# Optimization experiments

Hardware: AMD Instinct MI355X
Metric: run time of the kernel (lower is better)

The kernel has to match this reference:

```python
import jax, jax.numpy as jnp
import numpy as np


def setup_inputs() -> dict:
    key = jax.random.key(0)
    x = jax.random.normal(key, (4, 256, 64, 64), dtype=jnp.float32)
    return {"x": x}


def reference(x):
    # x: [B, C, W, H]
    B, C, W, H = x.shape
    N = W * H
    q = x.reshape(B, C, N).transpose(0, 2, 1)  # [B, N, C] (proj_query)
    # per-token L2 norm over channels
    q_norm = jnp.linalg.norm(q, ord=2, axis=2)  # [B, N]
    # outer product of norms: [B, N, N]
    nm = q_norm[:, :, None] * q_norm[:, None, :]
    # raw dot-product energy: [B, N, N]
    energy = jnp.einsum('bnc,bmc->bnm', q, q)
    norm_energy = energy / (nm + 1e-6)
    attention = jax.nn.softmax(norm_energy, axis=-1)
    return attention
```

## Files before the change

kernel.cpp:

```cpp
#include <hip/hip_runtime.h>
#include <hip/hip_bf16.h>

#define BATCH 4
#define CDIM  256
#define NTOK  4096

#define BM 64
#define BN 128

typedef short bf16x8 __attribute__((ext_vector_type(8)));
typedef float floatx4 __attribute__((ext_vector_type(4)));
typedef unsigned int uintx4 __attribute__((ext_vector_type(4)));
typedef unsigned int u32;

#define PIN(v) asm volatile("" : "+v"(v))
#define WAIT(n) asm volatile("s_waitcnt vmcnt(" #n ")" ::: "memory")
#define BAR() do { __builtin_amdgcn_s_barrier(); asm volatile("" ::: "memory"); } while (0)

__device__ inline u32 f2bf1(float f) {
    u32 u = __float_as_uint(f);
    u += 0x7fffu + ((u >> 16) & 1u);
    return u >> 16;
}
__device__ inline u32 f2bf2(float lo, float hi) { return f2bf1(lo) | (f2bf1(hi) << 16); }

__device__ inline void gload_lds16(const short* g, short* l) {
    __builtin_amdgcn_global_load_lds(
        (const __attribute__((address_space(1))) u32*)g,
        (__attribute__((address_space(3))) u32*)l, 16, 0, 0);
}

#define TT 32
__global__ __launch_bounds__(256) void prep_kernel(const float* __restrict__ x,
                                                   short* __restrict__ xn) {
    __shared__ float tile[TT][CDIM + 2];
    __shared__ float part[8][TT];
    __shared__ float rinv_s[TT];
    const int tid = threadIdx.x;
    const int blk = blockIdx.x;
    const int b = blk >> 7;
    const int t0 = (blk & 127) * TT;
    const float* xb = x + (size_t)b * CDIM * NTOK;
    const int ti = tid & 31, cq = tid >> 5;
    float ss = 0.f;
    for (int c = cq; c < CDIM; c += 8) {
        float v = xb[(size_t)c * NTOK + t0 + ti];
        tile[ti][c] = v;
        ss += v * v;
    }
    part[cq][ti] = ss;
    __syncthreads();
    if (tid < TT) {
        float s = 0.f;
#pragma unroll
        for (int q = 0; q < 8; ++q) s += part[q][tid];
        rinv_s[tid] = 1.0f / sqrtf(s);
    }
    __syncthreads();
    const int tok = tid >> 3, seg = tid & 7;
    const float ri = rinv_s[tok];
    size_t obase = ((size_t)(b * NTOK + t0 + tok)) * CDIM + seg * 32;
#pragma unroll
    for (int j = 0; j < 4; ++j) {
        u32 w[4];
#pragma unroll
        for (int u = 0; u < 4; ++u) {
            float f0 = tile[tok][seg * 32 + j * 8 + 2 * u] * ri;
            float f1 = tile[tok][seg * 32 + j * 8 + 2 * u + 1] * ri;
            w[u] = f2bf2(f0, f1);
        }
        *(uintx4*)&xn[obase + j * 8] = (uintx4){w[0], w[1], w[2], w[3]};
    }
}

__global__ __launch_bounds__(512, 2) void attn_kernel(const short* __restrict__ xn,
                                                      float* __restrict__ out) {
    __shared__ short Bs[4][128][64];
    __shared__ float rowsumLds[BM][4];
    const int tid = threadIdx.x;
    const int D = blockIdx.x;
    const int b = D >> 6;
    const int rb = (D & 63) * BM;
    const short* xnb = xn + (size_t)b * NTOK * CDIM;
    float* outb = out + ((size_t)b << 24);
    const int lane = tid & 63, wid = tid >> 6;
    const int wr = (wid >> 2) * 32;
    const int wc = (wid & 3) * 32;
    const int r0 = lane & 15, kq = lane >> 4;
    const int sx = r0 & 7;
    const int tr0 = wc + r0, tr1 = wc + 16 + r0;

    const int trl0 = (wid << 3) + (lane >> 3);
    const int c8 = (lane & 7) ^ (lane >> 3);

    bf16x8 afr[2][8];
#pragma unroll
    for (int m = 0; m < 2; ++m) {
        const short* arow = xnb + (size_t)(rb + wr + m * 16 + r0) * CDIM;
#pragma unroll
        for (int j = 0; j < 8; ++j) {
            afr[m][j] = *(const bf16x8*)(arow + j * 32 + kq * 8);
            PIN(afr[m][j]);
        }
    }

    float psum0[4] = {0.f, 0.f, 0.f, 0.f}, psum1[4] = {0.f, 0.f, 0.f, 0.f};
    float rinv0[4], rinv1[4];
    floatx4 acc00, acc01, acc10, acc11;

    auto stage = [&](int ct, int kc) {
        const short* s0 = xnb + (size_t)(ct * BN + trl0) * CDIM + kc * 64 + c8 * 8;
        short* d = &Bs[kc][wid << 3][0];
        gload_lds16(s0, d);
        gload_lds16(s0 + (size_t)64 * CDIM, d + 64 * 64);
    };

#define ACCZERO() do { acc00 = (floatx4){0,0,0,0}; acc01 = (floatx4){0,0,0,0}; \
                       acc10 = (floatx4){0,0,0,0}; acc11 = (floatx4){0,0,0,0}; } while (0)

#define COMPUTE(KC) do { \
    __builtin_amdgcn_s_setprio(1); \
    const int p0 = kq ^ sx, p1 = (4 | kq) ^ sx; \
    bf16x8 b0a = *(const bf16x8*)&Bs[KC][tr0][p0 * 8]; \
    bf16x8 b1a = *(const bf16x8*)&Bs[KC][tr1][p0 * 8]; \
    bf16x8 b0b = *(const bf16x8*)&Bs[KC][tr0][p1 * 8]; \
    bf16x8 b1b = *(const bf16x8*)&Bs[KC][tr1][p1 * 8]; \
    acc00 = __builtin_amdgcn_mfma_f32_16x16x32_bf16(afr[0][(KC)*2],   b0a, acc00, 0,0,0); \
    acc10 = __builtin_amdgcn_mfma_f32_16x16x32_bf16(afr[1][(KC)*2],   b0a, acc10, 0,0,0); \
    acc01 = __builtin_amdgcn_mfma_f32_16x16x32_bf16(afr[0][(KC)*2],   b1a, acc01, 0,0,0); \
    acc11 = __builtin_amdgcn_mfma_f32_16x16x32_bf16(afr[1][(KC)*2],   b1a, acc11, 0,0,0); \
    acc00 = __builtin_amdgcn_mfma_f32_16x16x32_bf16(afr[0][(KC)*2+1], b0b, acc00, 0,0,0); \
    acc10 = __builtin_amdgcn_mfma_f32_16x16x32_bf16(afr[1][(KC)*2+1], b0b, acc10, 0,0,0); \
    acc01 = __builtin_amdgcn_mfma_f32_16x16x32_bf16(afr[0][(KC)*2+1], b1b, acc01, 0,0,0); \
    acc11 = __builtin_amdgcn_mfma_f32_16x16x32_bf16(afr[1][(KC)*2+1], b1b, acc11, 0,0,0); \
    __builtin_amdgcn_s_setprio(0); \
} while (0)

#define STEP(KC, SCT, SKC, WN) do { stage((SCT), (SKC)); WAIT(WN); BAR(); COMPUTE(KC); } while (0)
#define STEPNS(KC, WN)        do { WAIT(WN); BAR(); COMPUTE(KC); } while (0)

#define EPI0() do { \
    _Pragma("unroll") for (int r = 0; r < 4; ++r) { \
        psum0[r] += __expf(acc00[r] - 1.f) + __expf(acc01[r] - 1.f); \
        psum1[r] += __expf(acc10[r] - 1.f) + __expf(acc11[r] - 1.f); } \
} while (0)

#define EPI1(CT) do { \
    _Pragma("unroll") for (int r = 0; r < 4; ++r) { \
        const int row_a = rb + wr + kq * 4 + r; \
        float* pa = outb + ((size_t)row_a << 12) + ((CT) << 7) + wc + r0; \
        __builtin_nontemporal_store(__expf(acc00[r] - 1.f) * rinv0[r], pa); \
        __builtin_nontemporal_store(__expf(acc01[r] - 1.f) * rinv0[r], pa + 16); \
        float* pb = pa + ((size_t)16 << 12); \
        __builtin_nontemporal_store(__expf(acc10[r] - 1.f) * rinv1[r], pb); \
        __builtin_nontemporal_store(__expf(acc11[r] - 1.f) * rinv1[r], pb + 16); } \
} while (0)

    stage(0, 0); stage(0, 1);
    for (int ct = 0; ct < 31; ++ct) {
        ACCZERO();
        STEP(0, ct, 2, 4);
        STEP(1, ct, 3, 4);
        STEP(2, ct + 1, 0, 4);
        STEP(3, ct + 1, 1, 4);
        EPI0();
    }
    ACCZERO();
    STEP(0, 31, 2, 4);
    STEP(1, 31, 3, 4);
    STEPNS(2, 2);
    STEPNS(3, 0);
    EPI0();

#pragma unroll
    for (int r = 0; r < 4; ++r) {
        float v0 = psum0[r], v1 = psum1[r];
        v0 += __shfl_xor(v0, 1); v0 += __shfl_xor(v0, 2);
        v0 += __shfl_xor(v0, 4); v0 += __shfl_xor(v0, 8);
        v1 += __shfl_xor(v1, 1); v1 += __shfl_xor(v1, 2);
        v1 += __shfl_xor(v1, 4); v1 += __shfl_xor(v1, 8);
        if (r0 == 0) {
            rowsumLds[wr + kq * 4 + r][wid & 3] = v0;
            rowsumLds[wr + 16 + kq * 4 + r][wid & 3] = v1;
        }
    }
    __syncthreads();
#pragma unroll
    for (int r = 0; r < 4; ++r) {
        const int ra = wr + kq * 4 + r, rbw = wr + 16 + kq * 4 + r;
        rinv0[r] = 1.0f / (rowsumLds[ra][0] + rowsumLds[ra][1] + rowsumLds[ra][2] + rowsumLds[ra][3]);
        rinv1[r] = 1.0f / (rowsumLds[rbw][0] + rowsumLds[rbw][1] + rowsumLds[rbw][2] + rowsumLds[rbw][3]);
    }
    __syncthreads();

    stage(0, 0); stage(0, 1);
    {
        ACCZERO();
        STEP(0, 0, 2, 4);
        STEP(1, 0, 3, 4);
        STEP(2, 1, 0, 4);
        STEP(3, 1, 1, 4);
        EPI1(0);
    }
    for (int ct = 1; ct < 31; ++ct) {
        ACCZERO();
        STEP(0, ct, 2, 12);
        STEP(1, ct, 3, 12);
        STEP(2, ct + 1, 0, 4);
        STEP(3, ct + 1, 1, 4);
        EPI1(ct);
    }
    ACCZERO();
    STEP(0, 31, 2, 12);
    STEP(1, 31, 3, 12);
    STEPNS(2, 2);
    STEPNS(3, 0);
    EPI1(31);

#undef ACCZERO
#undef COMPUTE
#undef STEP
#undef STEPNS
#undef EPI0
#undef EPI1
}

extern "C" void kernel_launch(void* const* d_in, const int* in_sizes, int n_in,
                              void* d_out, int out_size, void* d_ws, size_t ws_size,
                              hipStream_t stream) {
    const float* x = (const float*)d_in[0];
    float* out = (float*)d_out;
    short* xn = (short*)d_ws;

    prep_kernel<<<BATCH * (NTOK / TT), 256, 0, stream>>>(x, xn);
    attn_kernel<<<NTOK / BM * BATCH, 512, 0, stream>>>(xn, out);
}
```

Baseline: 143.8 us.

## Stage attention output through LDS for coalesced stores and defer the epilogue by one tile

The second pass now writes the normalized exp values into a padded LDS tile. After a barrier, each wave reads rows of that tile and writes them with 16-byte nontemporal vector stores, replacing the scattered 4-byte global stores. The epilogue for each column tile is delayed by one iteration, using saved accumulators, and placed between MFMA steps of the next tile. The vmcnt wait counts are adjusted to account for the extra stores. The new ~33 KB LDS buffer raises per-block LDS use considerably, which may limit how many blocks fit per CU. It also adds an extra barrier and LDS round-trip per tile.

```diff
diff --git a/kernel.cpp b/kernel.cpp
--- a/kernel.cpp
+++ b/kernel.cpp
@@ -15,6 +15,7 @@
 
 #define PIN(v) asm volatile("" : "+v"(v))
 #define WAIT(n) asm volatile("s_waitcnt vmcnt(" #n ")" ::: "memory")
+#define LGKM0() asm volatile("s_waitcnt lgkmcnt(0)" ::: "memory")
 #define BAR() do { __builtin_amdgcn_s_barrier(); asm volatile("" ::: "memory"); } while (0)
 
 __device__ inline u32 f2bf1(float f) {
@@ -76,6 +77,7 @@
 __global__ __launch_bounds__(512, 2) void attn_kernel(const short* __restrict__ xn,
                                                       float* __restrict__ out) {
     __shared__ short Bs[4][128][64];
+    __shared__ float Co[64][132];
     __shared__ float rowsumLds[BM][4];
     const int tid = threadIdx.x;
     const int D = blockIdx.x;
@@ -107,6 +109,7 @@
     float psum0[4] = {0.f, 0.f, 0.f, 0.f}, psum1[4] = {0.f, 0.f, 0.f, 0.f};
     float rinv0[4], rinv1[4];
     floatx4 acc00, acc01, acc10, acc11;
+    floatx4 accP00, accP01, accP10, accP11;
 
     auto stage = [&](int ct, int kc) {
         const short* s0 = xnb + (size_t)(ct * BN + trl0) * CDIM + kc * 64 + c8 * 8;
@@ -117,6 +120,7 @@
 
 #define ACCZERO() do { acc00 = (floatx4){0,0,0,0}; acc01 = (floatx4){0,0,0,0}; \
                        acc10 = (floatx4){0,0,0,0}; acc11 = (floatx4){0,0,0,0}; } while (0)
+#define SAVEACC() do { accP00 = acc00; accP01 = acc01; accP10 = acc10; accP11 = acc11; } while (0)
 
 #define COMPUTE(KC) do { \
     __builtin_amdgcn_s_setprio(1); \
@@ -145,15 +149,20 @@
         psum1[r] += __expf(acc10[r] - 1.f) + __expf(acc11[r] - 1.f); } \
 } while (0)
 
-#define EPI1(CT) do { \
+#define SP(CT) do { \
     _Pragma("unroll") for (int r = 0; r < 4; ++r) { \
-        const int row_a = rb + wr + kq * 4 + r; \
-        float* pa = outb + ((size_t)row_a << 12) + ((CT) << 7) + wc + r0; \
-        __builtin_nontemporal_store(__expf(acc00[r] - 1.f) * rinv0[r], pa); \
-        __builtin_nontemporal_store(__expf(acc01[r] - 1.f) * rinv0[r], pa + 16); \
-        float* pb = pa + ((size_t)16 << 12); \
-        __builtin_nontemporal_store(__expf(acc10[r] - 1.f) * rinv1[r], pb); \
-        __builtin_nontemporal_store(__expf(acc11[r] - 1.f) * rinv1[r], pb + 16); } \
+        const int rowa = wr + kq * 4 + r; \
+        Co[rowa][wc + r0]           = __expf(accP00[r] - 1.f) * rinv0[r]; \
+        Co[rowa][wc + 16 + r0]      = __expf(accP01[r] - 1.f) * rinv0[r]; \
+        Co[rowa + 16][wc + r0]      = __expf(accP10[r] - 1.f) * rinv1[r]; \
+        Co[rowa + 16][wc + 16 + r0] = __expf(accP11[r] - 1.f) * rinv1[r]; } \
+    LGKM0(); \
+    BAR(); \
+    _Pragma("unroll") for (int p = 0; p < 4; ++p) { \
+        const int rw = (wid << 3) + (lane >> 5) + 2 * p; \
+        floatx4 v = *(const floatx4*)&Co[rw][(lane & 31) * 4]; \
+        __builtin_nontemporal_store(v, \
+            (floatx4*)(outb + (((size_t)(rb + rw)) << 12) + ((CT) << 7) + (lane & 31) * 4)); } \
 } while (0)
 
     stage(0, 0); stage(0, 1);
@@ -194,35 +203,37 @@
     __syncthreads();
 
     stage(0, 0); stage(0, 1);
-    {
-        ACCZERO();
-        STEP(0, 0, 2, 4);
-        STEP(1, 0, 3, 4);
-        STEP(2, 1, 0, 4);
-        STEP(3, 1, 1, 4);
-        EPI1(0);
-    }
+    ACCZERO();
+    STEP(0, 0, 2, 4);
+    STEP(1, 0, 3, 4);
+    STEP(2, 1, 0, 4);
+    STEP(3, 1, 1, 4);
+    SAVEACC();
     for (int ct = 1; ct < 31; ++ct) {
         ACCZERO();
-        STEP(0, ct, 2, 12);
-        STEP(1, ct, 3, 12);
-        STEP(2, ct + 1, 0, 4);
-        STEP(3, ct + 1, 1, 4);
-        EPI1(ct);
+        STEP(0, ct, 2, 4);
+        STEP(1, ct, 3, 4);
+        SP(ct - 1);
+        STEP(2, ct + 1, 0, 8);
+        STEP(3, ct + 1, 1, 8);
+        SAVEACC();
     }
     ACCZERO();
-    STEP(0, 31, 2, 12);
-    STEP(1, 31, 3, 12);
-    STEPNS(2, 2);
-    STEPNS(3, 0);
-    EPI1(31);
+    STEP(0, 31, 2, 4);
+    STEP(1, 31, 3, 4);
+    SP(30);
+    STEPNS(2, 6);
+    STEPNS(3, 4);
+    SAVEACC();
+    SP(31);
 
 #undef ACCZERO
+#undef SAVEACC
 #undef COMPUTE
 #undef STEP
 #undef STEPNS
 #undef EPI0
-#undef EPI1
+#undef SP
 }
 
 extern "C" void kernel_launch(void* const* d_in, const int* in_sizes, int n_in,
```

After: 145.5 us. About the same (+1.2%).

## Widen column tile to 256 with 1x8 warp layout covering all rows

Applied to the files above, without the earlier changes.

Doubles the column tile (BN 128→256) and reorganizes the eight warps so each one covers all 64 rows and a 32-column slice. Each warp now holds four A row-fragments in registers, so every B fragment read from LDS feeds four MFMAs instead of two, and the number of column-tile iterations per pass is halved. The cost is a 128 KB LDS B buffer and twice as many A registers, which likely prevents two blocks per CU despite the launch bounds. The row-sum reduction now spans eight warps, and the vmcnt waits are retuned for the larger stage and store counts.

```diff
diff --git a/kernel.cpp b/kernel.cpp
--- a/kernel.cpp
+++ b/kernel.cpp
@@ -6,7 +6,7 @@
 #define NTOK  4096
 
 #define BM 64
-#define BN 128
+#define BN 256
 
 typedef short bf16x8 __attribute__((ext_vector_type(8)));
 typedef float floatx4 __attribute__((ext_vector_type(4)));
@@ -75,8 +75,8 @@
 
 __global__ __launch_bounds__(512, 2) void attn_kernel(const short* __restrict__ xn,
                                                       float* __restrict__ out) {
-    __shared__ short Bs[4][128][64];
-    __shared__ float rowsumLds[BM][4];
+    __shared__ short Bs[4][256][64];
+    __shared__ float rowsumLds[BM][8];
     const int tid = threadIdx.x;
     const int D = blockIdx.x;
     const int b = D >> 6;
@@ -84,19 +84,18 @@
     const short* xnb = xn + (size_t)b * NTOK * CDIM;
     float* outb = out + ((size_t)b << 24);
     const int lane = tid & 63, wid = tid >> 6;
-    const int wr = (wid >> 2) * 32;
-    const int wc = (wid & 3) * 32;
+    const int wcol = wid << 5;
     const int r0 = lane & 15, kq = lane >> 4;
     const int sx = r0 & 7;
-    const int tr0 = wc + r0, tr1 = wc + 16 + r0;
-
-    const int trl0 = (wid << 3) + (lane >> 3);
+    const int tr0 = wcol + r0, tr1 = wcol + 16 + r0;
+
+    const int trl = (wid << 3) + (lane >> 3);
     const int c8 = (lane & 7) ^ (lane >> 3);
 
-    bf16x8 afr[2][8];
-#pragma unroll
-    for (int m = 0; m < 2; ++m) {
-        const short* arow = xnb + (size_t)(rb + wr + m * 16 + r0) * CDIM;
+    bf16x8 afr[4][8];
+#pragma unroll
+    for (int m = 0; m < 4; ++m) {
+        const short* arow = xnb + (size_t)(rb + m * 16 + r0) * CDIM;
 #pragma unroll
         for (int j = 0; j < 8; ++j) {
             afr[m][j] = *(const bf16x8*)(arow + j * 32 + kq * 8);
@@ -104,35 +103,37 @@
         }
     }
 
-    float psum0[4] = {0.f, 0.f, 0.f, 0.f}, psum1[4] = {0.f, 0.f, 0.f, 0.f};
-    float rinv0[4], rinv1[4];
-    floatx4 acc00, acc01, acc10, acc11;
+    float psum[16];
+#pragma unroll
+    for (int i = 0; i < 16; ++i) psum[i] = 0.f;
+    floatx4 acc[4][2];
 
     auto stage = [&](int ct, int kc) {
-        const short* s0 = xnb + (size_t)(ct * BN + trl0) * CDIM + kc * 64 + c8 * 8;
+        const short* s0 = xnb + (size_t)(ct * BN + trl) * CDIM + kc * 64 + c8 * 8;
         short* d = &Bs[kc][wid << 3][0];
-        gload_lds16(s0, d);
-        gload_lds16(s0 + (size_t)64 * CDIM, d + 64 * 64);
+#pragma unroll
+        for (int rr = 0; rr < 4; ++rr)
+            gload_lds16(s0 + (size_t)(rr * 64) * CDIM, d + rr * 64 * 64);
     };
 
-#define ACCZERO() do { acc00 = (floatx4){0,0,0,0}; acc01 = (floatx4){0,0,0,0}; \
-                       acc10 = (floatx4){0,0,0,0}; acc11 = (floatx4){0,0,0,0}; } while (0)
+#define ACCZERO() do { _Pragma("unroll") for (int m = 0; m < 4; ++m) { \
+        acc[m][0] = (floatx4){0,0,0,0}; acc[m][1] = (floatx4){0,0,0,0}; } } while (0)
 
 #define COMPUTE(KC) do { \
     __builtin_amdgcn_s_setprio(1); \
     const int p0 = kq ^ sx, p1 = (4 | kq) ^ sx; \
-    bf16x8 b0a = *(const bf16x8*)&Bs[KC][tr0][p0 * 8]; \
-    bf16x8 b1a = *(const bf16x8*)&Bs[KC][tr1][p0 * 8]; \
-    bf16x8 b0b = *(const bf16x8*)&Bs[KC][tr0][p1 * 8]; \
-    bf16x8 b1b = *(const bf16x8*)&Bs[KC][tr1][p1 * 8]; \
-    acc00 = __builtin_amdgcn_mfma_f32_16x16x32_bf16(afr[0][(KC)*2],   b0a, acc00, 0,0,0); \
-    acc10 = __builtin_amdgcn_mfma_f32_16x16x32_bf16(afr[1][(KC)*2],   b0a, acc10, 0,0,0); \
-    acc01 = __builtin_amdgcn_mfma_f32_16x16x32_bf16(afr[0][(KC)*2],   b1a, acc01, 0,0,0); \
-    acc11 = __builtin_amdgcn_mfma_f32_16x16x32_bf16(afr[1][(KC)*2],   b1a, acc11, 0,0,0); \
-    acc00 = __builtin_amdgcn_mfma_f32_16x16x32_bf16(afr[0][(KC)*2+1], b0b, acc00, 0,0,0); \
-    acc10 = __builtin_amdgcn_mfma_f32_16x16x32_bf16(afr[1][(KC)*2+1], b0b, acc10, 0,0,0); \
-    acc01 = __builtin_amdgcn_mfma_f32_16x16x32_bf16(afr[0][(KC)*2+1], b1b, acc01, 0,0,0); \
-    acc11 = __builtin_amdgcn_mfma_f32_16x16x32_bf16(afr[1][(KC)*2+1], b1b, acc11, 0,0,0); \
+    bf16x8 b00 = *(const bf16x8*)&Bs[KC][tr0][p0 * 8]; \
+    bf16x8 b10 = *(const bf16x8*)&Bs[KC][tr1][p0 * 8]; \
+    bf16x8 b01 = *(const bf16x8*)&Bs[KC][tr0][p1 * 8]; \
+    bf16x8 b11 = *(const bf16x8*)&Bs[KC][tr1][p1 * 8]; \
+    _Pragma("unroll") for (int m = 0; m < 4; ++m) \
+        acc[m][0] = __builtin_amdgcn_mfma_f32_16x16x32_bf16(afr[m][(KC)*2], b00, acc[m][0], 0,0,0); \
+    _Pragma("unroll") for (int m = 0; m < 4; ++m) \
+        acc[m][1] = __builtin_amdgcn_mfma_f32_16x16x32_bf16(afr[m][(KC)*2], b10, acc[m][1], 0,0,0); \
+    _Pragma("unroll") for (int m = 0; m < 4; ++m) \
+        acc[m][0] = __builtin_amdgcn_mfma_f32_16x16x32_bf16(afr[m][(KC)*2+1], b01, acc[m][0], 0,0,0); \
+    _Pragma("unroll") for (int m = 0; m < 4; ++m) \
+        acc[m][1] = __builtin_amdgcn_mfma_f32_16x16x32_bf16(afr[m][(KC)*2+1], b11, acc[m][1], 0,0,0); \
     __builtin_amdgcn_s_setprio(0); \
 } while (0)
 
@@ -140,82 +141,82 @@
 #define STEPNS(KC, WN)        do { WAIT(WN); BAR(); COMPUTE(KC); } while (0)
 
 #define EPI0() do { \
+    _Pragma("unroll") for (int m = 0; m < 4; ++m) \
+    _Pragma("unroll") for (int r = 0; r < 4; ++r) \
+        psum[m * 4 + r] += __expf(acc[m][0][r] - 1.f) + __expf(acc[m][1][r] - 1.f); \
+} while (0)
+
+#define EPI1(CT) do { \
+    _Pragma("unroll") for (int m = 0; m < 4; ++m) \
     _Pragma("unroll") for (int r = 0; r < 4; ++r) { \
-        psum0[r] += __expf(acc00[r] - 1.f) + __expf(acc01[r] - 1.f); \
-        psum1[r] += __expf(acc10[r] - 1.f) + __expf(acc11[r] - 1.f); } \
+        const int row = rb + m * 16 + kq * 4 + r; \
+        float* p = outb + ((size_t)row << 12) + ((CT) << 8) + wcol + r0; \
+        const float ri = psum[m * 4 + r]; \
+        __builtin_nontemporal_store(__expf(acc[m][0][r] - 1.f) * ri, p); \
+        __builtin_nontemporal_store(__expf(acc[m][1][r] - 1.f) * ri, p + 16); } \
 } while (0)
 
-#define EPI1(CT) do { \
-    _Pragma("unroll") for (int r = 0; r < 4; ++r) { \
-        const int row_a = rb + wr + kq * 4 + r; \
-        float* pa = outb + ((size_t)row_a << 12) + ((CT) << 7) + wc + r0; \
-        __builtin_nontemporal_store(__expf(acc00[r] - 1.f) * rinv0[r], pa); \
-        __builtin_nontemporal_store(__expf(acc01[r] - 1.f) * rinv0[r], pa + 16); \
-        float* pb = pa + ((size_t)16 << 12); \
-        __builtin_nontemporal_store(__expf(acc10[r] - 1.f) * rinv1[r], pb); \
-        __builtin_nontemporal_store(__expf(acc11[r] - 1.f) * rinv1[r], pb + 16); } \
-} while (0)
-
     stage(0, 0); stage(0, 1);
-    for (int ct = 0; ct < 31; ++ct) {
+    for (int ct = 0; ct < 15; ++ct) {
         ACCZERO();
-        STEP(0, ct, 2, 4);
-        STEP(1, ct, 3, 4);
-        STEP(2, ct + 1, 0, 4);
-        STEP(3, ct + 1, 1, 4);
+        STEP(0, ct, 2, 8);
+        STEP(1, ct, 3, 8);
+        STEP(2, ct + 1, 0, 8);
+        STEP(3, ct + 1, 1, 8);
         EPI0();
     }
     ACCZERO();
-    STEP(0, 31, 2, 4);
-    STEP(1, 31, 3, 4);
-    STEPNS(2, 2);
+    STEP(0, 15, 2, 8);
+    STEP(1, 15, 3, 8);
+    STEPNS(2, 4);
     STEPNS(3, 0);
     EPI0();
 
 #pragma unroll
-    for (int r = 0; r < 4; ++r) {
-        float v0 = psum0[r], v1 = psum1[r];
-        v0 += __shfl_xor(v0, 1); v0 += __shfl_xor(v0, 2);
-        v0 += __shfl_xor(v0, 4); v0 += __shfl_xor(v0, 8);
-        v1 += __shfl_xor(v1, 1); v1 += __shfl_xor(v1, 2);
-        v1 += __shfl_xor(v1, 4); v1 += __shfl_xor(v1, 8);
-        if (r0 == 0) {
-            rowsumLds[wr + kq * 4 + r][wid & 3] = v0;
-            rowsumLds[wr + 16 + kq * 4 + r][wid & 3] = v1;
-        }
-    }
-    __syncthreads();
-#pragma unroll
-    for (int r = 0; r < 4; ++r) {
-        const int ra = wr + kq * 4 + r, rbw = wr + 16 + kq * 4 + r;
-        rinv0[r] = 1.0f / (rowsumLds[ra][0] + rowsumLds[ra][1] + rowsumLds[ra][2] + rowsumLds[ra][3]);
-        rinv1[r] = 1.0f / (rowsumLds[rbw][0] + rowsumLds[rbw][1] + rowsumLds[rbw][2] + rowsumLds[rbw][3]);
-    }
+    for (int m = 0; m < 4; ++m)
+#pragma unroll
+        for (int r = 0; r < 4; ++r) {
+            float v = psum[m * 4 + r];
+            v += __shfl_xor(v, 1); v += __shfl_xor(v, 2);
+            v += __shfl_xor(v, 4); v += __shfl_xor(v, 8);
+            if (r0 == 0) rowsumLds[m * 16 + kq * 4 + r][wid] = v;
+        }
+    __syncthreads();
+#pragma unroll
+    for (int m = 0; m < 4; ++m)
+#pragma unroll
+        for (int r = 0; r < 4; ++r) {
+            const int row = m * 16 + kq * 4 + r;
+            float s = 0.f;
+#pragma unroll
+            for (int w = 0; w < 8; ++w) s += rowsumLds[row][w];
+            psum[m * 4 + r] = 1.0f / s;
+        }
     __syncthreads();
 
     stage(0, 0); stage(0, 1);
     {
         ACCZERO();
-        STEP(0, 0, 2, 4);
-        STEP(1, 0, 3, 4);
-        STEP(2, 1, 0, 4);
-        STEP(3, 1, 1, 4);
+        STEP(0, 0, 2, 8);
+        STEP(1, 0, 3, 8);
+        STEP(2, 1, 0, 8);
+        STEP(3, 1, 1, 8);
         EPI1(0);
     }
-    for (int ct = 1; ct < 31; ++ct) {
+    for (int ct = 1; ct < 15; ++ct) {
         ACCZERO();
-        STEP(0, ct, 2, 12);
-        STEP(1, ct, 3, 12);
-        STEP(2, ct + 1, 0, 4);
-        STEP(3, ct + 1, 1, 4);
+        STEP(0, ct, 2, 40);
+        STEP(1, ct, 3, 40);
+        STEP(2, ct + 1, 0, 8);
+        STEP(3, ct + 1, 1, 8);
         EPI1(ct);
     }
     ACCZERO();
-    STEP(0, 31, 2, 12);
-    STEP(1, 31, 3, 12);
-    STEPNS(2, 2);
+    STEP(0, 15, 2, 40);
+    STEP(1, 15, 3, 40);
+    STEPNS(2, 4);
     STEPNS(3, 0);
-    EPI1(31);
+    EPI1(15);
 
 #undef ACCZERO
 #undef COMPUTE
```

Result: slower. 154.3 us (+7.3%).
